# Kernel tuning notes

Measured on AMD Instinct MI355X. Metric: run time of the kernel, lower is better.

The kernel has to match this reference:

```python
import math
import jax, jax.numpy as jnp
import numpy as np

ROUNDS = 4
BUCKET_LEN = 64
NEG_BIG = -1e9
NEG_SELF = -1e5
EPS = 1e-12


def look_back(x):
    # x: [B, n_buckets, bucket_len, ...]; prepend previous bucket (circular) along bucket_len axis
    return jnp.concatenate([jnp.roll(x, 1, axis=1), x], axis=2)


def gather_dim1(x, idx):
    # torch expand_gather: broadcast x and idx to common shape, gather along axis 1
    shape = np.broadcast_shapes(x.shape, idx.shape)
    return jnp.take_along_axis(jnp.broadcast_to(x, shape), jnp.broadcast_to(idx, shape), axis=1)


def setup_inputs() -> dict:
    key = jax.random.key(0)
    k1, k2, k3 = jax.random.split(key, 3)
    B, L, d_k = 16, 4096, 64
    n_buckets = L // BUCKET_LEN
    query = jax.random.normal(k1, (B, L, d_k), dtype=jnp.float32)
    value = jax.random.normal(k2, (B, L, d_k), dtype=jnp.float32)
    rand_matrix = jax.random.normal(k3, (B, d_k, ROUNDS, n_buckets // 2), dtype=jnp.float32)
    return {"query": query, "value": value, "rand_matrix": rand_matrix, "seed": 0}


def lsh_hashes(query, rand_matrix):
    # LocalitySensitiveHash.forward
    B, L, d_k = query.shape
    qn = query / jnp.maximum(jnp.linalg.norm(query, axis=-1, keepdims=True), EPS)
    rm = rand_matrix / jnp.linalg.norm(rand_matrix, axis=1, keepdims=True)
    mm = jnp.einsum('bld,bdrn->blrn', qn, rm)  # [B, L, rounds, n_buckets//2]
    h = jnp.argmax(jnp.concatenate([mm, -mm], axis=-1), axis=-1).astype(jnp.int32)  # [B, L, rounds]
    return h * L + jnp.arange(L, dtype=jnp.int32)[None, :, None]  # unique per position


def _lsh_attention(query, value, rand_matrix):
    B, L, d_k = query.shape
    R, bl = ROUNDS, BUCKET_LEN
    nb = L // bl

    h = lsh_hashes(query, rand_matrix)
    sorted_hashes = jnp.sort(h, axis=1)
    hash_indice = jnp.argsort(h, axis=1)               # [B, L, R]
    original_indice = jnp.argsort(hash_indice, axis=1)  # reverse_sort

    # reorder queries by hash, bucketize: [B, nb, bl, d_k, R]
    rq = gather_dim1(query[:, :, :, None], hash_indice[:, :, None, :]).reshape(B, nb, bl, d_k, R)
    lb_key = look_back(rq)
    lb_key = lb_key / jnp.maximum(jnp.linalg.norm(lb_key, axis=-2, keepdims=True), EPS)
    scores = jnp.einsum('bnidr,bnjdr->bnijr', rq, lb_key) / math.sqrt(d_k)  # [B, nb, bl, 2bl, R]

    # mask: different buckets, causal, self
    sh = sorted_hashes.reshape(B, nb, bl, R) // L  # bucket id
    scores = jnp.where(sh[..., None, :] != look_back(sh)[..., None, :, :], NEG_BIG, scores)
    qi = hash_indice.reshape(B, nb, bl, R).astype(jnp.int32)
    ki = look_back(qi)  # [B, nb, 2bl, R]
    scores = jnp.where(qi[..., None, :] < ki[..., None, :, :], NEG_BIG, scores)
    scores = jnp.where(qi[..., None, :] == ki[..., None, :, :], NEG_SELF, scores)

    # duplicate-key counting across rounds (get_dup_keys)
    ki_full = jnp.broadcast_to(ki[:, :, None, :, :], (B, nb, bl, 2 * bl, R)).reshape(B, L, 2 * bl, R)
    ki_full = gather_dim1(ki_full, original_indice[:, :, None, :])
    flat = ki_full.reshape(B, L, 2 * bl * R)
    s_idx = jnp.argsort(flat, axis=-1)
    s = jnp.take_along_axis(flat, s_idx, axis=-1)
    counts = jnp.ones_like(s)
    for i in range(1, R):
        eq = (s[..., i:] == s[..., :-i]).astype(s.dtype)
        counts = counts + jnp.pad(eq, ((0, 0), (0, 0), (i, 0))) + jnp.pad(eq, ((0, 0), (0, 0), (0, i)))
    inv = jnp.argsort(s_idx, axis=-1)
    count_key = jnp.take_along_axis(counts, inv, axis=-1).reshape(B, L, 2 * bl, R)
    count_key = gather_dim1(count_key, hash_indice[:, :, None, :])

    # duplicate-adjusted softmax
    scores = scores.reshape(B, L, 2 * bl, R)
    lse = jax.nn.logsumexp(scores, axis=2)  # [B, L, R]
    softmax_qk = jnp.exp(scores - jnp.log(count_key.astype(scores.dtype)) - lse[:, :, None, :])

    rv = gather_dim1(value[:, :, :, None], hash_indice[:, :, None, :]).reshape(B, nb, bl, d_k, R)
    sm = softmax_qk.reshape(B, nb, bl, 2 * bl, R)
    attn = jnp.einsum('bnijr,bnjdr->bnidr', sm, look_back(rv)).reshape(B, L, d_k, R)
    attn = gather_dim1(attn, original_indice[:, :, None, :])
    lse = jnp.take_along_axis(lse, original_indice, axis=1)
    round_weights = jax.nn.softmax(lse, axis=1)  # dim=1 (length) exactly as in the source
    return jnp.einsum('bldr,blr->bld', attn, round_weights)


def reference(query, value, rand_matrix, seed):
    # seed is unused by the original forward body; dropout skipped (eval mode)
    return _lsh_attention(query, value, rand_matrix)
```

## Files before the change

kernel.cpp:

```cpp
#include <hip/hip_runtime.h>
#include <math.h>

#define B_  16
#define L_  4096
#define D_  64
#define R_  4
#define NB_ 64
#define BL_ 64
#define FIXCAP 8192

typedef _Float16 f16x8 __attribute__((ext_vector_type(8)));
typedef _Float16 f16x2 __attribute__((ext_vector_type(2)));
typedef float    f32x4 __attribute__((ext_vector_type(4)));


__global__ __launch_bounds__(64) void k_rmnorm(const float* __restrict__ rm,
                                               double* __restrict__ rmn,
                                               _Float16* __restrict__ rhi_g,
                                               _Float16* __restrict__ rlo_g,
                                               int* __restrict__ fix_cnt) {
    if (blockIdx.x == 0 && threadIdx.x == 0) *fix_cnt = 0;
    int blk = blockIdx.x;
    int b = blk >> 7, r = (blk >> 5) & 3, n = blk & 31;
    int d = threadIdx.x;
    double v = (double)rm[(((size_t)b * 64 + d) * 4 + r) * 32 + n];
    double sq = v * v;
    #pragma unroll
    for (int off = 32; off > 0; off >>= 1) sq += __shfl_down(sq, off);
    double tot = __shfl(sq, 0);
    double nv = v / sqrt(tot);
    rmn[(((size_t)b * 4 + r) * 32 + n) * 64 + d] = nv;
    float f = (float)nv;
    _Float16 hi = (_Float16)f;
    size_t gi = ((size_t)b * 128 + r * 32 + n) * 64 + d;
    rhi_g[gi] = hi;
    rlo_g[gi] = (_Float16)(f - (float)hi);
}

__global__ __launch_bounds__(256, 4) void k_hash(const float* __restrict__ q,
                                                 const float* __restrict__ value,
                                                 const _Float16* __restrict__ rhi_g,
                                                 const _Float16* __restrict__ rlo_g,
                                                 int* __restrict__ h_ws,
                                                 int* __restrict__ fix_cnt,
                                                 int* __restrict__ fix_list,
                                                 float* __restrict__ qscale_g,
                                                 _Float16* __restrict__ khf,
                                                 _Float16* __restrict__ vhf) {
    __shared__ __align__(16) char smem[36864];
    _Float16* Rhi = (_Float16*)smem;
    _Float16* Rlo = (_Float16*)(smem + 18432);
    float*    Sc  = (float*)smem;

    int blk = blockIdx.x;
    int b = blk >> 6, chunk = blk & 63;
    int tid = threadIdx.x;
    int w = tid >> 6, lane = tid & 63, quad = lane >> 4, l15 = lane & 15;

    {
        int row = chunk * 64 + (tid >> 2), sub = tid & 3;
        const float4* vp = (const float4*)(value + ((size_t)(b * L_ + row)) * 64 + sub * 16);
        f16x8 h0, h1;
        #pragma unroll
        for (int c = 0; c < 2; c++) {
            float4 t0 = vp[2 * c], t1 = vp[2 * c + 1];
            f16x8& hd = c ? h1 : h0;
            hd[0]=(_Float16)t0.x; hd[1]=(_Float16)t0.y; hd[2]=(_Float16)t0.z; hd[3]=(_Float16)t0.w;
            hd[4]=(_Float16)t1.x; hd[5]=(_Float16)t1.y; hd[6]=(_Float16)t1.z; hd[7]=(_Float16)t1.w;
        }
        _Float16* dst = vhf + ((size_t)(b * L_ + row)) * 64 + sub * 16;
        *(f16x8*)dst = h0;
        *(f16x8*)(dst + 8) = h1;
    }

    {
        int row = tid >> 1, dh = (tid & 1) * 32;
        const _Float16* sh = rhi_g + ((size_t)b * 128 + row) * 64 + dh;
        const _Float16* sl = rlo_g + ((size_t)b * 128 + row) * 64 + dh;
        #pragma unroll
        for (int g = 0; g < 4; g++) {
            *(f16x8*)&Rhi[row * 72 + dh + g * 8] = *(const f16x8*)(sh + g * 8);
            *(f16x8*)&Rlo[row * 72 + dh + g * 8] = *(const f16x8*)(sl + g * 8);
        }
    }

    int qrow = chunk * 64 + w * 16 + l15;
    const float* qp = q + ((size_t)(b * L_ + qrow)) * 64;
    float qv[16];
    #pragma unroll
    for (int kt = 0; kt < 2; kt++) {
        float4 t0 = *(const float4*)(qp + kt * 32 + quad * 8);
        float4 t1 = *(const float4*)(qp + kt * 32 + quad * 8 + 4);
        qv[8*kt+0]=t0.x; qv[8*kt+1]=t0.y; qv[8*kt+2]=t0.z; qv[8*kt+3]=t0.w;
        qv[8*kt+4]=t1.x; qv[8*kt+5]=t1.y; qv[8*kt+6]=t1.z; qv[8*kt+7]=t1.w;
    }
    f16x8 Ahi[2], Alo[2];
    #pragma unroll
    for (int kt = 0; kt < 2; kt++) {
        #pragma unroll
        for (int j = 0; j < 8; j++) {
            _Float16 hi = (_Float16)qv[8*kt+j];
            Ahi[kt][j] = hi;
            Alo[kt][j] = (_Float16)(qv[8*kt+j] - (float)hi);
        }
    }
    {
        float ss = 0.f;
        #pragma unroll
        for (int j = 0; j < 16; j++) ss += qv[j] * qv[j];
        ss += __shfl_xor(ss, 16);
        ss += __shfl_xor(ss, 32);
        float nr = sqrtf(ss); if (nr < 1e-12f) nr = 1e-12f;
        float kscale = 0.18033688f / nr;
        if (quad == 0) qscale_g[(size_t)b * L_ + qrow] = nr * 5.5451774445f;
        _Float16* kd = khf + ((size_t)(b * L_ + qrow)) * 64;
        #pragma unroll
        for (int kt = 0; kt < 2; kt++) {
            f16x8 hv;
            #pragma unroll
            for (int j = 0; j < 8; j++) hv[j] = (_Float16)(qv[8*kt+j] * kscale);
            *(f16x8*)(kd + kt * 32 + quad * 8) = hv;
        }
    }
    __syncthreads();

    f32x4 acc[8];
    #pragma unroll
    for (int jt = 0; jt < 8; jt++) acc[jt] = (f32x4){0.f, 0.f, 0.f, 0.f};
    #pragma unroll
    for (int jt = 0; jt < 8; jt++) {
        #pragma unroll
        for (int kt = 0; kt < 2; kt++) {
            f16x8 bh = *(const f16x8*)&Rhi[(jt * 16 + l15) * 72 + kt * 32 + quad * 8];
            f16x8 bl = *(const f16x8*)&Rlo[(jt * 16 + l15) * 72 + kt * 32 + quad * 8];
            acc[jt] = __builtin_amdgcn_mfma_f32_16x16x32_f16(Ahi[kt], bh, acc[jt], 0, 0, 0);
            acc[jt] = __builtin_amdgcn_mfma_f32_16x16x32_f16(Ahi[kt], bl, acc[jt], 0, 0, 0);
            acc[jt] = __builtin_amdgcn_mfma_f32_16x16x32_f16(Alo[kt], bh, acc[jt], 0, 0, 0);
        }
    }
    __syncthreads();

    #pragma unroll
    for (int jt = 0; jt < 8; jt++) {
        #pragma unroll
        for (int reg = 0; reg < 4; reg++)
            Sc[(w * 16 + quad * 4 + reg) * 133 + jt * 16 + l15] = acc[jt][reg];
    }
    __syncthreads();

    {
        int row = tid & 63, r = tid >> 6;
        const float* sp = &Sc[row * 133 + r * 32];
        float v1 = -1e30f, v2 = -1e30f; int i1 = 0;
        #pragma unroll
        for (int n = 0; n < 32; n++) {
            float v = sp[n];
            float a = fabsf(v);
            int cand = n | ((__float_as_uint(v) >> 26) & 32);
            if (a > v1) i1 = cand;
            v2 = __builtin_amdgcn_fmed3f(a, v1, v2);
            v1 = fmaxf(a, v1);
        }
        int l = chunk * 64 + row;
        h_ws[((size_t)(b * 4 + r)) * L_ + l] = i1;
        if (v1 - v2 < 4e-5f) {
            int slot = atomicAdd(fix_cnt, 1);
            if (slot < FIXCAP) fix_list[slot] = (b << 14) | (r << 12) | l;
        }
    }
}

__global__ __launch_bounds__(64) void k_fix(const float* __restrict__ q,
                                            const double* __restrict__ rmn,
                                            const int* __restrict__ fix_cnt,
                                            const int* __restrict__ fix_list,
                                            int* __restrict__ h_ws) {
    int cnt = *fix_cnt; if (cnt > FIXCAP) cnt = FIXCAP;
    int lane = threadIdx.x;
    for (int i = blockIdx.x; i < cnt; i += gridDim.x) {
        int e = fix_list[i];
        int b = e >> 14, r = (e >> 12) & 3, l = e & 4095;
        int n = lane & 31;
        const double* rp = rmn + ((size_t)(b * 4 + r)) * 2048 + n * 64;
        const float* qr = q + ((size_t)(b * L_ + l)) * 64;
        double a0 = 0.0, a1 = 0.0, a2 = 0.0, a3 = 0.0;
        #pragma unroll
        for (int d = 0; d < 64; d += 4) {
            a0 += (double)qr[d]   * rp[d];
            a1 += (double)qr[d+1] * rp[d+1];
            a2 += (double)qr[d+2] * rp[d+2];
            a3 += (double)qr[d+3] * rp[d+3];
        }
        double acc = ((a0 + a1) + (a2 + a3));
        double v = (lane < 32) ? acc : -acc;
        int idx = lane;
        #pragma unroll
        for (int off = 1; off < 64; off <<= 1) {
            double ov = __shfl_xor(v, off);
            int   oidx = __shfl_xor(idx, off);
            if (ov > v || (ov == v && oidx < idx)) { v = ov; idx = oidx; }
        }
        if (lane == 0) h_ws[((size_t)(b * 4 + r)) * L_ + l] = idx;
    }
}

__global__ __launch_bounds__(256) void k_sort(const int* __restrict__ h_ws,
                                              int* __restrict__ oi_ws,
                                              int* __restrict__ bstart_g) {
    __shared__ __align__(16) unsigned short cnt[64 * 257];
    __shared__ __align__(16) unsigned short oi_s[256 * 17];
    __shared__ int part[256];

    int br = blockIdx.x;
    int t = threadIdx.x;
    const int* hp = h_ws + (size_t)br * L_;

    unsigned int* cz = (unsigned int*)cnt;
    #pragma unroll
    for (int i = 0; i < 33; i++) {
        int idx = i * 256 + t;
        if (idx < 8224) cz[idx] = 0;
    }

    int key[16];
    const int4* hp4 = (const int4*)(hp + t * 16);
    #pragma unroll
    for (int g = 0; g < 4; g++) {
        int4 v = hp4[g];
        key[g*4+0] = v.x; key[g*4+1] = v.y; key[g*4+2] = v.z; key[g*4+3] = v.w;
    }
    __syncthreads();

    #pragma unroll
    for (int k = 0; k < 16; k++) {
        unsigned short* c = &cnt[key[k] * 257 + t];
        *c = (unsigned short)(*c + 1);
    }
    __syncthreads();

    int u = t & 63, s = t >> 6;
    {
        int run = 0;
        int base_idx = u * 257 + s * 64;
        #pragma unroll 16
        for (int i = 0; i < 64; i++) {
            int c = cnt[base_idx + i];
            cnt[base_idx + i] = (unsigned short)run;
            run += c;
        }
        part[s * 64 + u] = run;
    }
    __syncthreads();

    if (t < 64) {
        int p0 = part[t], p1 = part[64 + t], p2 = part[128 + t], p3 = part[192 + t];
        int tot = p0 + p1 + p2 + p3;
        int v = tot;
        #pragma unroll
        for (int off = 1; off < 64; off <<= 1) {
            int o = __shfl_up(v, off);
            if (t >= off) v += o;
        }
        int base = v - tot;
        bstart_g[br * 64 + t] = base;
        part[t]       = base;
        part[64 + t]  = base + p0;
        part[128 + t] = base + p0 + p1;
        part[192 + t] = base + p0 + p1 + p2;
    }
    __syncthreads();

    int sbase = s * 64;
    #pragma unroll
    for (int k = 0; k < 16; k++) {
        int uk = key[k];
        unsigned short* c = &cnt[uk * 257 + t];
        int pos = part[sbase + uk] + *c;
        *c = (unsigned short)(*c + 1);
        int idx = t * 16 + k;
        oi_s[(idx >> 4) * 17 + (idx & 15)] = (unsigned short)pos;
    }
    __syncthreads();

    int* op = oi_ws + (size_t)br * L_;
    #pragma unroll
    for (int k = 0; k < 16; k++) {
        int e = k * 256 + t;
        op[e] = (int)oi_s[(e >> 4) * 17 + (e & 15)];
    }
}

__global__ __launch_bounds__(256) void k_meta(const int* __restrict__ h_ws,
                                              const int* __restrict__ oi_ws,
                                              const int* __restrict__ bstart_g,
                                              int4* __restrict__ meta_ws) {
    int gid = blockIdx.x * 256 + threadIdx.x;
    int br = gid >> 12, p = gid & 4095;
    int b = br >> 2, rme = br & 3;
    int hh = h_ws[(size_t)br * L_ + p];
    int pack = 0, packm1 = 0, mypos = 0;
    #pragma unroll
    for (int r2 = 0; r2 < 4; r2++) {
        int o = oi_ws[((size_t)(b * 4 + r2)) * L_ + p];
        if (r2 == rme) mypos = o;
        int bk = o >> 6;
        pack   |= bk << (8 * r2);
        packm1 |= ((bk + 63) & 63) << (8 * r2);
    }
    int sb = bstart_g[br * 64 + hh];
    meta_ws[(size_t)br * L_ + mypos] = make_int4(sb, p, pack, packm1);
}

__global__ __launch_bounds__(256, 4) void k_attn(const float* __restrict__ qscale_g,
                                                 const _Float16* __restrict__ khf,
                                                 const _Float16* __restrict__ vhf,
                                                 const int4* __restrict__ meta_ws,
                                                 float* __restrict__ lse_ws,
                                                 _Float16* __restrict__ attn_ws) {
    __shared__ _Float16 Ksh[128 * 72];
    __shared__ _Float16 Vt[64 * 136];
    __shared__ int4 kmeta[128];

    int xcd = blockIdx.x & 7, slot = blockIdx.x >> 3;
    int b = xcd * 2 + (slot >> 8);
    int rem = slot & 255, n = rem >> 2, r = rem & 3;
    int tid = threadIdx.x;
    int w = tid >> 6, lane = tid & 63, quad = lane >> 4, l15 = lane & 15;
    int hibase = (b * 4 + r) * L_;
    const int4* mp = meta_ws + hibase;
    int nprev = (n + 63) & 63;

    {
        int j = tid >> 1, dh = (tid & 1) * 32;
        int spos = (j < 64) ? (nprev * 64 + j) : (n * 64 + (j - 64));
        int4 me = mp[spos];
        if (dh == 0) kmeta[j] = me;
        const _Float16* src = khf + ((size_t)(b * L_ + me.y)) * 64 + dh;
        #pragma unroll
        for (int g = 0; g < 4; g++)
            *(f16x8*)&Ksh[j * 72 + dh + g * 8] = *(const f16x8*)(src + g * 8);
    }
    __syncthreads();

    {
        int m = tid >> 2, sub = tid & 3;
        int y0 = kmeta[2 * m].y, y1 = kmeta[2 * m + 1].y;
        const _Float16* v0 = vhf + ((size_t)(b * L_ + y0)) * 64 + sub * 16;
        const _Float16* v1 = vhf + ((size_t)(b * L_ + y1)) * 64 + sub * 16;
        f16x8 a00 = *(const f16x8*)v0, a01 = *(const f16x8*)(v0 + 8);
        f16x8 a10 = *(const f16x8*)v1, a11 = *(const f16x8*)(v1 + 8);
        #pragma unroll
        for (int d = 0; d < 8; d++) {
            f16x2 hv = { a00[d], a10[d] };
            *(f16x2*)&Vt[(sub * 16 + d) * 136 + 2 * m] = hv;
            f16x2 hw = { a01[d], a11[d] };
            *(f16x2*)&Vt[(sub * 16 + 8 + d) * 136 + 2 * m] = hw;
        }
    }

    f16x8 afr[2];
    afr[0] = *(const f16x8*)&Ksh[(64 + w * 16 + l15) * 72 + quad * 8];
    afr[1] = *(const f16x8*)&Ksh[(64 + w * 16 + l15) * 72 + 32 + quad * 8];

    f32x4 acc[8];
    #pragma unroll
    for (int jt = 0; jt < 8; jt++) acc[jt] = (f32x4){0.f, 0.f, 0.f, 0.f};
    __builtin_amdgcn_s_setprio(1);
    #pragma unroll
    for (int jt = 0; jt < 8; jt++) {
        #pragma unroll
        for (int kt = 0; kt < 2; kt++) {
            f16x8 bfr = *(const f16x8*)&Ksh[(jt * 16 + l15) * 72 + kt * 32 + quad * 8];
            acc[jt] = __builtin_amdgcn_mfma_f32_16x16x32_f16(afr[kt], bfr, acc[jt], 0, 0, 0);
        }
    }
    __builtin_amdgcn_s_setprio(0);

    int4 qm4[4]; int km4z[8]; float qs4[4];
    #pragma unroll
    for (int reg = 0; reg < 4; reg++) {
        qm4[reg] = kmeta[64 + w * 16 + quad * 4 + reg];
        qs4[reg] = qscale_g[(size_t)b * L_ + qm4[reg].y];
    }
    #pragma unroll
    for (int jt = 0; jt < 8; jt++) km4z[jt] = kmeta[jt * 16 + l15].z;
    __syncthreads();

    _Float16* Ph = Ksh;
    float lse_r[4], inv_r[4];
    #pragma unroll
    for (int reg = 0; reg < 4; reg++) {
        int lo = qm4[reg].x - (n - 1) * 64;
        int width = w * 16 + quad * 4 + reg + 64 - lo;
        int jl = l15 - lo;
        float qs = qs4[reg];
        float s[8];
        #pragma unroll
        for (int jt = 0; jt < 8; jt++) {
            float v = acc[jt][reg] * qs;
            int ju = jt * 16 + jl;
            v = ((unsigned)ju < (unsigned)width) ? v : -1.4426951e9f;
            if (ju == width) v = -144269.50f;
            s[jt] = v;
        }
        float m = s[0];
        #pragma unroll
        for (int jt = 1; jt < 8; jt++) m = fmaxf(m, s[jt]);
        #pragma unroll
        for (int off = 1; off < 16; off <<= 1) m = fmaxf(m, __shfl_xor(m, off));
        float te[8], sum = 0.f;
        #pragma unroll
        for (int jt = 0; jt < 8; jt++) { te[jt] = __builtin_amdgcn_exp2f(s[jt] - m); sum += te[jt]; }
        #pragma unroll
        for (int off = 1; off < 16; off <<= 1) sum += __shfl_xor(sum, off);
        inv_r[reg] = __builtin_amdgcn_rcpf(sum);
        lse_r[reg] = m * 0.6931472f + __logf(sum);
        int i = w * 16 + quad * 4 + reg;
        #pragma unroll
        for (int jt = 0; jt < 8; jt++) {
            int z1 = km4z[jt] ^ qm4[reg].z;
            int z2 = km4z[jt] ^ qm4[reg].w;
            int nz = __popc((z1 + 0x7f7f7f7f) & 0x80808080)
                   + __popc((z2 + 0x7f7f7f7f) & 0x80808080);
            float p = te[jt] * __builtin_amdgcn_rcpf((float)(8 - nz));
            Ph[i * 136 + jt * 16 + l15] = (_Float16)p;
        }
    }
    if (l15 == 0) {
        #pragma unroll
        for (int reg = 0; reg < 4; reg++)
            lse_ws[hibase + qm4[reg].y] = lse_r[reg];
    }
    __syncthreads();

    f32x4 oacc[4];
    #pragma unroll
    for (int nt = 0; nt < 4; nt++) oacc[nt] = (f32x4){0.f, 0.f, 0.f, 0.f};
    __builtin_amdgcn_s_setprio(1);
    #pragma unroll
    for (int kt = 0; kt < 4; kt++) {
        f16x8 pa = *(const f16x8*)&Ph[(w * 16 + l15) * 136 + kt * 32 + quad * 8];
        #pragma unroll
        for (int nt = 0; nt < 4; nt++) {
            f16x8 vb = *(const f16x8*)&Vt[(nt * 16 + l15) * 136 + kt * 32 + quad * 8];
            oacc[nt] = __builtin_amdgcn_mfma_f32_16x16x32_f16(pa, vb, oacc[nt], 0, 0, 0);
        }
    }
    __builtin_amdgcn_s_setprio(0);
    __syncthreads();

    _Float16* Pout = Ksh;
    #pragma unroll
    for (int nt = 0; nt < 4; nt++) {
        #pragma unroll
        for (int reg = 0; reg < 4; reg++) {
            int i = w * 16 + quad * 4 + reg;
            Pout[i * 72 + nt * 16 + l15] = (_Float16)(oacc[nt][reg] * inv_r[reg]);
        }
    }
    __syncthreads();

    {
        int row = tid >> 2, part = tid & 3;
        int y = kmeta[64 + row].y;
        _Float16* dst = attn_ws + ((size_t)hibase + y) * 64;
        f16x8 v0 = *(const f16x8*)&Pout[row * 72 + part * 8];
        f16x8 v1 = *(const f16x8*)&Pout[row * 72 + 32 + part * 8];
        *(f16x8*)(dst + part * 8) = v0;
        *(f16x8*)(dst + 32 + part * 8) = v1;
    }
}

__global__ __launch_bounds__(256) void k_rw(const float* __restrict__ lse_ws,
                                            float* __restrict__ rwmax,
                                            float* __restrict__ rwsum) {
    __shared__ float  red[256];
    __shared__ double redd[256];
    int br = blockIdx.x;
    const float* lp = lse_ws + (size_t)br * L_;
    int t = threadIdx.x;
    float m = -1e30f;
    for (int k = t; k < L_; k += 256) m = fmaxf(m, lp[k]);
    red[t] = m; __syncthreads();
    for (int s2 = 128; s2 > 0; s2 >>= 1) {
        if (t < s2) red[t] = fmaxf(red[t], red[t + s2]);
        __syncthreads();
    }
    float mm = red[0];
    double s = 0.0;
    for (int k = t; k < L_; k += 256) s += (double)expf(lp[k] - mm);
    redd[t] = s; __syncthreads();
    for (int s2 = 128; s2 > 0; s2 >>= 1) {
        if (t < s2) redd[t] += redd[t + s2];
        __syncthreads();
    }
    if (t == 0) { rwmax[br] = mm; rwsum[br] = (float)redd[0]; }
}

__global__ __launch_bounds__(256) void k_out(const _Float16* __restrict__ attn_ws,
                                             const float* __restrict__ lse_ws,
                                             const float* __restrict__ rwmax,
                                             const float* __restrict__ rwsum,
                                             float* __restrict__ out) {
    int gid = blockIdx.x * 256 + threadIdx.x;
    int g = gid & 7;
    size_t row = (size_t)(gid >> 3);
    int b = (int)(row >> 12), l = (int)(row & 4095);
    float o[8];
    #pragma unroll
    for (int k = 0; k < 8; k++) o[k] = 0.f;
    #pragma unroll
    for (int r = 0; r < 4; r++) {
        int br = b * 4 + r;
        float wgt = __expf(lse_ws[(size_t)br * L_ + l] - rwmax[br])
                  * __builtin_amdgcn_rcpf(rwsum[br]);
        f16x8 av = *(const f16x8*)&attn_ws[(((size_t)br * L_ + l) << 6) + g * 8];
        #pragma unroll
        for (int k = 0; k < 8; k++) o[k] += (float)av[k] * wgt;
    }
    float4* op = (float4*)(out + row * 64 + g * 8);
    op[0] = make_float4(o[0], o[1], o[2], o[3]);
    op[1] = make_float4(o[4], o[5], o[6], o[7]);
}

extern "C" void kernel_launch(void* const* d_in, const int* in_sizes, int n_in,
                              void* d_out, int out_size, void* d_ws, size_t ws_size,
                              hipStream_t stream) {
    const float* query = (const float*)d_in[0];
    const float* value = (const float*)d_in[1];
    const float* rm    = (const float*)d_in[2];
    char* ws = (char*)d_ws;
    double*    rmn    = (double*)ws;
    int*       h_ws   = (int*)(ws + ((size_t)1 << 20));
    int*       oi_ws  = (int*)(ws + ((size_t)3 << 20));
    float*     lse_ws = (float*)(ws + ((size_t)4 << 20));
    float*     rwmax  = (float*)(ws + ((size_t)5 << 20));
    float*     rwsum  = (float*)(ws + ((size_t)5 << 20) + 256);
    int*       fix_cnt= (int*)(ws + ((size_t)5 << 20) + 512);
    int*       fix_list=(int*)(ws + ((size_t)5 << 20) + 1024);
    int*       bstart = (int*)(ws + ((size_t)5 << 20) + ((size_t)256 << 10));
    _Float16*  attn_ws= (_Float16*)(ws + ((size_t)6 << 20));
    _Float16*  rhi_g  = (_Float16*)(ws + ((size_t)40 << 20));
    _Float16*  rlo_g  = (_Float16*)(ws + ((size_t)40 << 20) + ((size_t)1 << 19));
    int4*      meta_ws= (int4*)(ws + ((size_t)41 << 20));
    float*     qscale = (float*)(ws + ((size_t)45 << 20));
    _Float16*  khf    = (_Float16*)(ws + ((size_t)53 << 20));
    _Float16*  vhf    = (_Float16*)(ws + ((size_t)61 << 20));
    float*     out    = (float*)d_out;

    hipLaunchKernelGGL(k_rmnorm, dim3(2048), dim3(64),  0, stream, rm, rmn, rhi_g, rlo_g, fix_cnt);
    hipLaunchKernelGGL(k_hash,   dim3(1024), dim3(256), 0, stream, query, value, rhi_g, rlo_g,
                       h_ws, fix_cnt, fix_list, qscale, khf, vhf);
    hipLaunchKernelGGL(k_fix,    dim3(64),   dim3(64),  0, stream, query, rmn,
                       fix_cnt, fix_list, h_ws);
    hipLaunchKernelGGL(k_sort,   dim3(64),   dim3(256), 0, stream, h_ws, oi_ws, bstart);
    hipLaunchKernelGGL(k_meta,   dim3(1024), dim3(256), 0, stream, h_ws, oi_ws, bstart, meta_ws);
    hipLaunchKernelGGL(k_attn,   dim3(4096), dim3(256), 0, stream,
                       qscale, khf, vhf, meta_ws, lse_ws, attn_ws);
    hipLaunchKernelGGL(k_rw,     dim3(64),   dim3(256), 0, stream, lse_ws, rwmax, rwsum);
    hipLaunchKernelGGL(k_out,    dim3(2048), dim3(256), 0, stream,
                       attn_ws, lse_ws, rwmax, rwsum, out);
}
```

Baseline: 160.2 us.

## Fold rand-matrix normalization into hash, emit sorted metadata from sort kernel

Removes the k_rmnorm kernel. Each hash block now normalizes the random matrix in float and splits it into hi/lo halves itself, and k_fix recomputes the norm in double from the raw matrix. The sort kernel writes per-position bucket-start and source-index metadata directly, and a smaller k_pack kernel emits only the cross-round bucket packs, which k_attn gathers separately. The metadata loads in k_attn are also hoisted above the MFMA loop. The aim is fewer launches and less intermediate traffic, at the cost of redundant normalization per hash block, strided rm reads, and a float-precision norm in the fast path.

Measured after the change: 160.1 us. No clear change (-0.1%).

```diff
diff --git a/kernel.cpp b/kernel.cpp
--- a/kernel.cpp
+++ b/kernel.cpp
@@ -14,33 +14,9 @@
 typedef float    f32x4 __attribute__((ext_vector_type(4)));
 
 
-__global__ __launch_bounds__(64) void k_rmnorm(const float* __restrict__ rm,
-                                               double* __restrict__ rmn,
-                                               _Float16* __restrict__ rhi_g,
-                                               _Float16* __restrict__ rlo_g,
-                                               int* __restrict__ fix_cnt) {
-    if (blockIdx.x == 0 && threadIdx.x == 0) *fix_cnt = 0;
-    int blk = blockIdx.x;
-    int b = blk >> 7, r = (blk >> 5) & 3, n = blk & 31;
-    int d = threadIdx.x;
-    double v = (double)rm[(((size_t)b * 64 + d) * 4 + r) * 32 + n];
-    double sq = v * v;
-    #pragma unroll
-    for (int off = 32; off > 0; off >>= 1) sq += __shfl_down(sq, off);
-    double tot = __shfl(sq, 0);
-    double nv = v / sqrt(tot);
-    rmn[(((size_t)b * 4 + r) * 32 + n) * 64 + d] = nv;
-    float f = (float)nv;
-    _Float16 hi = (_Float16)f;
-    size_t gi = ((size_t)b * 128 + r * 32 + n) * 64 + d;
-    rhi_g[gi] = hi;
-    rlo_g[gi] = (_Float16)(f - (float)hi);
-}
-
 __global__ __launch_bounds__(256, 4) void k_hash(const float* __restrict__ q,
                                                  const float* __restrict__ value,
-                                                 const _Float16* __restrict__ rhi_g,
-                                                 const _Float16* __restrict__ rlo_g,
+                                                 const float* __restrict__ rm,
                                                  int* __restrict__ h_ws,
                                                  int* __restrict__ fix_cnt,
                                                  int* __restrict__ fix_list,
@@ -74,13 +50,25 @@
     }
 
     {
-        int row = tid >> 1, dh = (tid & 1) * 32;
-        const _Float16* sh = rhi_g + ((size_t)b * 128 + row) * 64 + dh;
-        const _Float16* sl = rlo_g + ((size_t)b * 128 + row) * 64 + dh;
-        #pragma unroll
-        for (int g = 0; g < 4; g++) {
-            *(f16x8*)&Rhi[row * 72 + dh + g * 8] = *(const f16x8*)(sh + g * 8);
-            *(f16x8*)&Rlo[row * 72 + dh + g * 8] = *(const f16x8*)(sl + g * 8);
+        int row = tid >> 1, dh2 = (tid & 1) * 32;
+        int rr = row >> 5, nn = row & 31;
+        const float* rpb = rm + (size_t)b * 8192 + rr * 32 + nn;
+        float ss = 0.f;
+        #pragma unroll
+        for (int g = 0; g < 32; g++) { float v = rpb[(dh2 + g) * 128]; ss += v * v; }
+        ss += __shfl_xor(ss, 1);
+        float rn = 1.0f / sqrtf(ss);
+        #pragma unroll
+        for (int gg = 0; gg < 4; gg++) {
+            f16x8 hv, lv;
+            #pragma unroll
+            for (int e = 0; e < 8; e++) {
+                float f = rpb[(dh2 + gg * 8 + e) * 128] * rn;
+                _Float16 h = (_Float16)f;
+                hv[e] = h; lv[e] = (_Float16)(f - (float)h);
+            }
+            *(f16x8*)&Rhi[row * 72 + dh2 + gg * 8] = hv;
+            *(f16x8*)&Rlo[row * 72 + dh2 + gg * 8] = lv;
         }
     }
 
@@ -171,7 +159,7 @@
 }
 
 __global__ __launch_bounds__(64) void k_fix(const float* __restrict__ q,
-                                            const double* __restrict__ rmn,
+                                            const float* __restrict__ rm,
                                             const int* __restrict__ fix_cnt,
                                             const int* __restrict__ fix_list,
                                             int* __restrict__ h_ws) {
@@ -181,17 +169,16 @@
         int e = fix_list[i];
         int b = e >> 14, r = (e >> 12) & 3, l = e & 4095;
         int n = lane & 31;
-        const double* rp = rmn + ((size_t)(b * 4 + r)) * 2048 + n * 64;
+        const float* rpb = rm + (size_t)b * 8192 + r * 32 + n;
         const float* qr = q + ((size_t)(b * L_ + l)) * 64;
-        double a0 = 0.0, a1 = 0.0, a2 = 0.0, a3 = 0.0;
-        #pragma unroll
-        for (int d = 0; d < 64; d += 4) {
-            a0 += (double)qr[d]   * rp[d];
-            a1 += (double)qr[d+1] * rp[d+1];
-            a2 += (double)qr[d+2] * rp[d+2];
-            a3 += (double)qr[d+3] * rp[d+3];
-        }
-        double acc = ((a0 + a1) + (a2 + a3));
+        double s2 = 0.0, dot = 0.0;
+        #pragma unroll 8
+        for (int d = 0; d < 64; d++) {
+            double m = (double)rpb[d * 128];
+            s2 += m * m;
+            dot += (double)qr[d] * m;
+        }
+        double acc = dot / sqrt(s2);
         double v = (lane < 32) ? acc : -acc;
         int idx = lane;
         #pragma unroll
@@ -206,10 +193,13 @@
 
 __global__ __launch_bounds__(256) void k_sort(const int* __restrict__ h_ws,
                                               int* __restrict__ oi_ws,
-                                              int* __restrict__ bstart_g) {
+                                              int2* __restrict__ metaA) {
     __shared__ __align__(16) unsigned short cnt[64 * 257];
     __shared__ __align__(16) unsigned short oi_s[256 * 17];
+    __shared__ __align__(16) unsigned short p_s[4096];
+    __shared__ __align__(16) unsigned short sb_s[4096];
     __shared__ int part[256];
+    __shared__ int bstart_s[64];
 
     int br = blockIdx.x;
     int t = threadIdx.x;
@@ -262,7 +252,7 @@
             if (t >= off) v += o;
         }
         int base = v - tot;
-        bstart_g[br * 64 + t] = base;
+        bstart_s[t] = base;
         part[t]       = base;
         part[64 + t]  = base + p0;
         part[128 + t] = base + p0 + p1;
@@ -279,42 +269,41 @@
         *c = (unsigned short)(*c + 1);
         int idx = t * 16 + k;
         oi_s[(idx >> 4) * 17 + (idx & 15)] = (unsigned short)pos;
+        p_s[pos]  = (unsigned short)idx;
+        sb_s[pos] = (unsigned short)bstart_s[uk];
     }
     __syncthreads();
 
     int* op = oi_ws + (size_t)br * L_;
+    int2* mp = metaA + (size_t)br * L_;
     #pragma unroll
     for (int k = 0; k < 16; k++) {
         int e = k * 256 + t;
         op[e] = (int)oi_s[(e >> 4) * 17 + (e & 15)];
-    }
-}
-
-__global__ __launch_bounds__(256) void k_meta(const int* __restrict__ h_ws,
-                                              const int* __restrict__ oi_ws,
-                                              const int* __restrict__ bstart_g,
-                                              int4* __restrict__ meta_ws) {
+        mp[e] = make_int2((int)sb_s[e], (int)p_s[e]);
+    }
+}
+
+__global__ __launch_bounds__(256) void k_pack(const int* __restrict__ oi_ws,
+                                              int2* __restrict__ packA) {
     int gid = blockIdx.x * 256 + threadIdx.x;
-    int br = gid >> 12, p = gid & 4095;
-    int b = br >> 2, rme = br & 3;
-    int hh = h_ws[(size_t)br * L_ + p];
-    int pack = 0, packm1 = 0, mypos = 0;
+    int b = gid >> 12, p = gid & 4095;
+    int pack = 0, packm1 = 0;
     #pragma unroll
     for (int r2 = 0; r2 < 4; r2++) {
         int o = oi_ws[((size_t)(b * 4 + r2)) * L_ + p];
-        if (r2 == rme) mypos = o;
         int bk = o >> 6;
         pack   |= bk << (8 * r2);
         packm1 |= ((bk + 63) & 63) << (8 * r2);
     }
-    int sb = bstart_g[br * 64 + hh];
-    meta_ws[(size_t)br * L_ + mypos] = make_int4(sb, p, pack, packm1);
+    packA[gid] = make_int2(pack, packm1);
 }
 
 __global__ __launch_bounds__(256, 4) void k_attn(const float* __restrict__ qscale_g,
                                                  const _Float16* __restrict__ khf,
                                                  const _Float16* __restrict__ vhf,
-                                                 const int4* __restrict__ meta_ws,
+                                                 const int2* __restrict__ metaA,
+                                                 const int2* __restrict__ packA,
                                                  float* __restrict__ lse_ws,
                                                  _Float16* __restrict__ attn_ws) {
     __shared__ _Float16 Ksh[128 * 72];
@@ -327,18 +316,26 @@
     int tid = threadIdx.x;
     int w = tid >> 6, lane = tid & 63, quad = lane >> 4, l15 = lane & 15;
     int hibase = (b * 4 + r) * L_;
-    const int4* mp = meta_ws + hibase;
+    const int2* mpA = metaA + hibase;
     int nprev = (n + 63) & 63;
 
     {
         int j = tid >> 1, dh = (tid & 1) * 32;
         int spos = (j < 64) ? (nprev * 64 + j) : (n * 64 + (j - 64));
-        int4 me = mp[spos];
-        if (dh == 0) kmeta[j] = me;
-        const _Float16* src = khf + ((size_t)(b * L_ + me.y)) * 64 + dh;
-        #pragma unroll
-        for (int g = 0; g < 4; g++)
-            *(f16x8*)&Ksh[j * 72 + dh + g * 8] = *(const f16x8*)(src + g * 8);
+        int2 ma = mpA[spos];
+        const _Float16* src = khf + ((size_t)(b * L_ + ma.y)) * 64 + dh;
+        f16x8 t0 = *(const f16x8*)(src);
+        f16x8 t1 = *(const f16x8*)(src + 8);
+        f16x8 t2 = *(const f16x8*)(src + 16);
+        f16x8 t3 = *(const f16x8*)(src + 24);
+        if (dh == 0) {
+            int2 pk = packA[b * L_ + ma.y];
+            kmeta[j] = make_int4(ma.x, ma.y, pk.x, pk.y);
+        }
+        *(f16x8*)&Ksh[j * 72 + dh + 0]  = t0;
+        *(f16x8*)&Ksh[j * 72 + dh + 8]  = t1;
+        *(f16x8*)&Ksh[j * 72 + dh + 16] = t2;
+        *(f16x8*)&Ksh[j * 72 + dh + 24] = t3;
     }
     __syncthreads();
 
@@ -362,6 +359,15 @@
     afr[0] = *(const f16x8*)&Ksh[(64 + w * 16 + l15) * 72 + quad * 8];
     afr[1] = *(const f16x8*)&Ksh[(64 + w * 16 + l15) * 72 + 32 + quad * 8];
 
+    int4 qm4[4]; int km4z[8]; float qs4[4];
+    #pragma unroll
+    for (int reg = 0; reg < 4; reg++) {
+        qm4[reg] = kmeta[64 + w * 16 + quad * 4 + reg];
+        qs4[reg] = qscale_g[(size_t)b * L_ + qm4[reg].y];
+    }
+    #pragma unroll
+    for (int jt = 0; jt < 8; jt++) km4z[jt] = kmeta[jt * 16 + l15].z;
+
     f32x4 acc[8];
     #pragma unroll
     for (int jt = 0; jt < 8; jt++) acc[jt] = (f32x4){0.f, 0.f, 0.f, 0.f};
@@ -375,15 +381,6 @@
         }
     }
     __builtin_amdgcn_s_setprio(0);
-
-    int4 qm4[4]; int km4z[8]; float qs4[4];
-    #pragma unroll
-    for (int reg = 0; reg < 4; reg++) {
-        qm4[reg] = kmeta[64 + w * 16 + quad * 4 + reg];
-        qs4[reg] = qscale_g[(size_t)b * L_ + qm4[reg].y];
-    }
-    #pragma unroll
-    for (int jt = 0; jt < 8; jt++) km4z[jt] = kmeta[jt * 16 + l15].z;
     __syncthreads();
 
     _Float16* Ph = Ksh;
@@ -530,7 +527,6 @@
     const float* value = (const float*)d_in[1];
     const float* rm    = (const float*)d_in[2];
     char* ws = (char*)d_ws;
-    double*    rmn    = (double*)ws;
     int*       h_ws   = (int*)(ws + ((size_t)1 << 20));
     int*       oi_ws  = (int*)(ws + ((size_t)3 << 20));
     float*     lse_ws = (float*)(ws + ((size_t)4 << 20));
@@ -538,25 +534,23 @@
     float*     rwsum  = (float*)(ws + ((size_t)5 << 20) + 256);
     int*       fix_cnt= (int*)(ws + ((size_t)5 << 20) + 512);
     int*       fix_list=(int*)(ws + ((size_t)5 << 20) + 1024);
-    int*       bstart = (int*)(ws + ((size_t)5 << 20) + ((size_t)256 << 10));
     _Float16*  attn_ws= (_Float16*)(ws + ((size_t)6 << 20));
-    _Float16*  rhi_g  = (_Float16*)(ws + ((size_t)40 << 20));
-    _Float16*  rlo_g  = (_Float16*)(ws + ((size_t)40 << 20) + ((size_t)1 << 19));
-    int4*      meta_ws= (int4*)(ws + ((size_t)41 << 20));
+    int2*      metaA  = (int2*)(ws + ((size_t)41 << 20));
+    int2*      packA  = (int2*)(ws + ((size_t)43 << 20));
     float*     qscale = (float*)(ws + ((size_t)45 << 20));
     _Float16*  khf    = (_Float16*)(ws + ((size_t)53 << 20));
     _Float16*  vhf    = (_Float16*)(ws + ((size_t)61 << 20));
     float*     out    = (float*)d_out;
 
-    hipLaunchKernelGGL(k_rmnorm, dim3(2048), dim3(64),  0, stream, rm, rmn, rhi_g, rlo_g, fix_cnt);
-    hipLaunchKernelGGL(k_hash,   dim3(1024), dim3(256), 0, stream, query, value, rhi_g, rlo_g,
+    hipMemsetAsync(fix_cnt, 0, sizeof(int), stream);
+    hipLaunchKernelGGL(k_hash,   dim3(1024), dim3(256), 0, stream, query, value, rm,
                        h_ws, fix_cnt, fix_list, qscale, khf, vhf);
-    hipLaunchKernelGGL(k_fix,    dim3(64),   dim3(64),  0, stream, query, rmn,
+    hipLaunchKernelGGL(k_fix,    dim3(64),   dim3(64),  0, stream, query, rm,
                        fix_cnt, fix_list, h_ws);
-    hipLaunchKernelGGL(k_sort,   dim3(64),   dim3(256), 0, stream, h_ws, oi_ws, bstart);
-    hipLaunchKernelGGL(k_meta,   dim3(1024), dim3(256), 0, stream, h_ws, oi_ws, bstart, meta_ws);
+    hipLaunchKernelGGL(k_sort,   dim3(64),   dim3(256), 0, stream, h_ws, oi_ws, metaA);
+    hipLaunchKernelGGL(k_pack,   dim3(256),  dim3(256), 0, stream, oi_ws, packA);
     hipLaunchKernelGGL(k_attn,   dim3(4096), dim3(256), 0, stream,
-                       qscale, khf, vhf, meta_ws, lse_ws, attn_ws);
+                       qscale, khf, vhf, metaA, packA, lse_ws, attn_ws);
     hipLaunchKernelGGL(k_rw,     dim3(64),   dim3(256), 0, stream, lse_ws, rwmax, rwsum);
     hipLaunchKernelGGL(k_out,    dim3(2048), dim3(256), 0, stream,
                        attn_ws, lse_ws, rwmax, rwsum, out);
```
